# Kernel optimization log

Measured on AMD Instinct MI355X. Metric: run time of the kernel, lower is better.

Reference implementation:

```python
import jax, jax.numpy as jnp
import numpy as np

B, S, E, H, V = 1024, 64, 100, 512, 50000


def _gru_backward_last(x, wih, whh, bih, bhh):
    # x: [B,S,E]; PyTorch GRU cell, reverse direction; return final hidden [B,H]
    def step(h, xt):
        gi = xt @ wih.T + bih          # [B,3H]
        gh = h @ whh.T + bhh           # [B,3H]
        ir, iz, i_n = jnp.split(gi, 3, axis=-1)
        hr, hz, h_n = jnp.split(gh, 3, axis=-1)
        r = jax.nn.sigmoid(ir + hr)
        z = jax.nn.sigmoid(iz + hz)
        n = jnp.tanh(i_n + r * h_n)
        return (1.0 - z) * n + z * h, None
    h0 = jnp.zeros((x.shape[0], whh.shape[1]), x.dtype)
    hT, _ = jax.lax.scan(step, h0, x.transpose(1, 0, 2), reverse=True)
    return hT


def _encode(tokens, emb, wih, whh, bih, bhh):
    return _gru_backward_last(emb[tokens], wih, whh, bih, bhh)


def setup_inputs() -> dict:
    key = jax.random.key(0)
    ks = jax.random.split(key, 32)
    d = {}
    d['query'] = jax.random.randint(ks[0], (B, S), 0, V)
    d['context'] = jax.random.randint(ks[1], (B, S), 0, V)
    d['reply'] = jax.random.randint(ks[2], (B, S), 0, V)
    i = 3
    for tag in ('q', 'c', 'r'):
        d[f'emb_{tag}'] = jax.random.uniform(ks[i], (V, E), jnp.float32, -0.25, 0.25); i += 1
        d[f'wih_{tag}'] = jax.random.normal(ks[i], (3 * H, E), jnp.float32) * 0.05; i += 1
        d[f'whh_{tag}'] = jax.random.normal(ks[i], (3 * H, H), jnp.float32) * 0.05; i += 1
        d[f'bih_{tag}'] = jnp.zeros((3 * H,), jnp.float32); i += 1
        d[f'bhh_{tag}'] = jnp.zeros((3 * H,), jnp.float32); i += 1
    d['lin_w'] = jax.random.normal(ks[i], (H, H), jnp.float32) * 0.02
    d['lin_b'] = jnp.zeros((H,), jnp.float32)
    return d


def reference(query, context, reply,
              emb_q, wih_q, whh_q, bih_q, bhh_q,
              emb_c, wih_c, whh_c, bih_c, bhh_c,
              emb_r, wih_r, whh_r, bih_r, bhh_r,
              lin_w, lin_b):
    eq = _encode(query, emb_q, wih_q, whh_q, bih_q, bhh_q)    # [B,H]
    ec = _encode(context, emb_c, wih_c, whh_c, bih_c, bhh_c)  # [B,H]
    er = _encode(reply, emb_r, wih_r, whh_r, bih_r, bhh_r)    # [B,H]
    eqc = ((eq + ec) * 0.5) @ lin_w.T + lin_b                  # [B,H]
    sim = lambda a: jax.nn.softmax(a @ er.T, axis=-1)          # [B,B]
    return sim(eq), sim(ec), sim(eqc)
```

## Files before the change

kernel.cpp:

```cpp
#include <hip/hip_runtime.h>

typedef unsigned short u16;
typedef __attribute__((ext_vector_type(8))) short short8;
typedef __attribute__((ext_vector_type(4))) float f32x4;

#define B_   1024
#define S_   64
#define E_   100
#define H_   512
#define G3_  1536
#define XW_  256
#define WSZG (32 * 3 * 40 * 512)
#define GS_  (40 * 512)

__device__ __forceinline__ float bf2f(u16 u) {
    union { unsigned int u; float f; } c; c.u = ((unsigned int)u) << 16; return c.f;
}
__device__ __forceinline__ u16 f2bf(float f) {
    union { float f; unsigned int u; } c; c.f = f;
    unsigned int r = c.u + 0x7fffu + ((c.u >> 16) & 1u);
    return (u16)(r >> 16);
}
__device__ __forceinline__ f32x4 mfma16(short8 a, short8 b, f32x4 c) {
    return __builtin_amdgcn_mfma_f32_16x16x32_bf16(a, b, c, 0, 0, 0);
}

__global__ __launch_bounds__(256) void gather_kernel(
    const int* __restrict__ tok, const float* __restrict__ emb, u16* __restrict__ xs)
{
    int tid = threadIdx.x;
    int hw  = tid & 31;
    int rowid = blockIdx.x * 8 + (tid >> 5);
    int t = rowid >> 10, b = rowid & 1023;
    int token = tok[b * S_ + t];
    const float* src = emb + (long)token * E_;
    u16* dst = xs + (long)rowid * XW_;
    int c0 = hw * 4;
    u16 a1[4], a2[4];
    #pragma unroll
    for (int j = 0; j < 4; ++j) {
        int c = c0 + j;
        float v = (c < E_) ? src[c] : 0.f;
        u16 h = f2bf(v);
        a1[j] = h;
        a2[j] = f2bf(v - bf2f(h));
    }
    uint2 p1, p2;
    p1.x = (unsigned)a1[0] | ((unsigned)a1[1] << 16);
    p1.y = (unsigned)a1[2] | ((unsigned)a1[3] << 16);
    p2.x = (unsigned)a2[0] | ((unsigned)a2[1] << 16);
    p2.y = (unsigned)a2[2] | ((unsigned)a2[3] << 16);
    *(uint2*)(dst + c0)       = p1;
    *(uint2*)(dst + 128 + c0) = p2;
}

__global__ __launch_bounds__(256) void repack_swz(
    const float* __restrict__ wih, const float* __restrict__ whh, u16* __restrict__ out)
{
    long idx = (long)blockIdx.x * 256 + threadIdx.x;
    int jj   = idx & 7;
    int lane = (idx >> 3) & 63;
    int q9   = (int)(idx >> 9);
    int ks   = q9 % 40;
    int q    = q9 / 40;
    int gate = q % 3;
    int ht   = q / 3;
    int n   = ht * 16 + (lane & 15);
    int ck  = (lane >> 4) * 8 + jj;
    int row = gate * H_ + n;
    float w; int lo;
    if (ks < 8) {
        int kk = (ks & 3) * 32 + ck;
        if (kk >= E_) { out[idx] = 0; return; }
        w = wih[row * E_ + kk];
        lo = (ks >> 2);
    } else {
        int rel = ks - 8;
        int kk  = (rel & 15) * 32 + ck;
        w = whh[row * H_ + kk];
        lo = (rel >> 4);
    }
    u16 h = f2bf(w);
    if (lo) h = f2bf(w - bf2f(h));
    out[idx] = h;
}

__global__ __launch_bounds__(256) void repack_lin(
    const float* __restrict__ lw, u16* __restrict__ l1, u16* __restrict__ l2)
{
    int i = blockIdx.x * 256 + threadIdx.x;
    float w = lw[i];
    u16 h = f2bf(w);
    l1[i] = h;
    l2[i] = f2bf(w - bf2f(h));
}

struct BiasPtrs { const float* bih[3]; const float* bhh[3]; };

__global__ __launch_bounds__(256, 3) void gru_step(
    const u16* __restrict__ xs,
    const u16* __restrict__ wswz,
    BiasPtrs bp,
    const u16* __restrict__ h1_in, const u16* __restrict__ h2_in,
    u16* __restrict__ h1_out, u16* __restrict__ h2_out,
    int t)
{
    __shared__ __attribute__((aligned(16))) u16 As[2 * 64 * 72];
    const int tid = threadIdx.x;
    const int lane = tid & 63;
    const int kh = tid >> 7;
    const int nh = (tid >> 6) & 1;
    const int l15 = lane & 15, l4 = lane >> 4;
    const int htp = blockIdx.x;
    const int m0  = blockIdx.y * 64;
    const int g   = blockIdx.z;
    const int ht  = htp * 2 + nh;

    const u16* wg  = wswz + (long)g * WSZG + (long)ht * (3 * GS_) + lane * 8;
    const u16* xb  = xs + ((long)(g * S_ + t) * B_ + m0) * XW_;
    const u16* hb1 = h1_in + ((long)g * B_ + m0) * H_;
    const u16* hb2 = h2_in + ((long)g * B_ + m0) * H_;
    u16* slotp = As + kh * (64 * 72);

    f32x4 zero = {0.f, 0.f, 0.f, 0.f};
    f32x4 acc_r[4]  = {zero, zero, zero, zero};
    f32x4 acc_z[4]  = {zero, zero, zero, zero};
    f32x4 acc_ni[4] = {zero, zero, zero, zero};
    f32x4 acc_nh[4] = {zero, zero, zero, zero};

    auto stage2 = [&](const u16* s0, const u16* s1, int stride) {
        #pragma unroll
        for (int i = 0; i < 2; ++i) {
            int s = tid + 256 * i;
            int row = s >> 3, seg = s & 7;
            *(uint4*)(&As[row * 72 + seg * 8]) =
                *(const uint4*)(s0 + (long)row * stride + seg * 8);
            *(uint4*)(&As[64 * 72 + row * 72 + seg * 8]) =
                *(const uint4*)(s1 + (long)row * stride + seg * 8);
        }
    };
    auto consume_dual = [&](const u16* b1, const u16* b2, f32x4* accn) {
        #pragma unroll
        for (int ksl = 0; ksl < 2; ++ksl) {
            short8 br1 = *(const short8*)(b1 + ksl * 512);
            short8 bz1 = *(const short8*)(b1 + GS_ + ksl * 512);
            short8 bn1 = *(const short8*)(b1 + 2 * GS_ + ksl * 512);
            short8 br2 = *(const short8*)(b2 + ksl * 512);
            short8 bz2 = *(const short8*)(b2 + GS_ + ksl * 512);
            short8 bn2 = *(const short8*)(b2 + 2 * GS_ + ksl * 512);
            short8 a[4];
            #pragma unroll
            for (int q = 0; q < 4; ++q)
                a[q] = *(const short8*)(&slotp[(q * 16 + l15) * 72 + ksl * 32 + l4 * 8]);
            #pragma unroll
            for (int q = 0; q < 4; ++q) {
                acc_r[q] = mfma16(a[q], br1, acc_r[q]);
                acc_z[q] = mfma16(a[q], bz1, acc_z[q]);
                accn[q]  = mfma16(a[q], bn1, accn[q]);
                acc_r[q] = mfma16(a[q], br2, acc_r[q]);
                acc_z[q] = mfma16(a[q], bz2, acc_z[q]);
                accn[q]  = mfma16(a[q], bn2, accn[q]);
            }
        }
    };
    auto consume_single = [&](const u16* b1, f32x4* accn) {
        #pragma unroll
        for (int ksl = 0; ksl < 2; ++ksl) {
            short8 br1 = *(const short8*)(b1 + ksl * 512);
            short8 bz1 = *(const short8*)(b1 + GS_ + ksl * 512);
            short8 bn1 = *(const short8*)(b1 + 2 * GS_ + ksl * 512);
            short8 a[4];
            #pragma unroll
            for (int q = 0; q < 4; ++q)
                a[q] = *(const short8*)(&slotp[(q * 16 + l15) * 72 + ksl * 32 + l4 * 8]);
            #pragma unroll
            for (int q = 0; q < 4; ++q) {
                acc_r[q] = mfma16(a[q], br1, acc_r[q]);
                acc_z[q] = mfma16(a[q], bz1, acc_z[q]);
                accn[q]  = mfma16(a[q], bn1, accn[q]);
            }
        }
    };

    stage2(xb, xb + 64, XW_);
    __syncthreads();
    consume_dual(wg + (2 * kh) * 512, wg + (4 + 2 * kh) * 512, acc_ni);
    __syncthreads();
    stage2(xb + 128, xb + 192, XW_);
    __syncthreads();
    consume_single(wg + (2 * kh) * 512, acc_ni);
    __syncthreads();
    #pragma unroll 1
    for (int i = 0; i < 4; ++i) {
        stage2(hb1 + i * 64, hb1 + (i + 4) * 64, H_);
        __syncthreads();
        consume_dual(wg + (8 + 8 * kh + 2 * i) * 512,
                     wg + (24 + 8 * kh + 2 * i) * 512, acc_nh);
        __syncthreads();
    }
    #pragma unroll 1
    for (int i = 0; i < 4; ++i) {
        stage2(hb2 + i * 64, hb2 + (i + 4) * 64, H_);
        __syncthreads();
        consume_single(wg + (8 + 8 * kh + 2 * i) * 512, acc_nh);
        __syncthreads();
    }

    f32x4* rp = (f32x4*)As;
    const int ridx = (nh * 64 + lane) * 8;
    if (kh == 1) {
        #pragma unroll
        for (int q = 0; q < 4; ++q) { rp[ridx + q] = acc_r[q]; rp[ridx + 4 + q] = acc_z[q]; }
    }
    __syncthreads();
    if (kh == 0) {
        #pragma unroll
        for (int q = 0; q < 4; ++q) { acc_r[q] += rp[ridx + q]; acc_z[q] += rp[ridx + 4 + q]; }
    }
    __syncthreads();
    if (kh == 1) {
        #pragma unroll
        for (int q = 0; q < 4; ++q) { rp[ridx + q] = acc_ni[q]; rp[ridx + 4 + q] = acc_nh[q]; }
    }
    __syncthreads();
    if (kh == 0) {
        #pragma unroll
        for (int q = 0; q < 4; ++q) { acc_ni[q] += rp[ridx + q]; acc_nh[q] += rp[ridx + 4 + q]; }

        int hc = ht * 16 + l15;
        const float* bih = bp.bih[g];
        const float* bhh = bp.bhh[g];
        float b_ir = bih[hc],          b_hr = bhh[hc];
        float b_iz = bih[H_ + hc],     b_hz = bhh[H_ + hc];
        float b_in = bih[2 * H_ + hc], b_hn = bhh[2 * H_ + hc];
        #pragma unroll
        for (int mt = 0; mt < 4; ++mt) {
            #pragma unroll
            for (int i = 0; i < 4; ++i) {
                int m = m0 + mt * 16 + l4 * 4 + i;
                long idx = ((long)g * B_ + m) * H_ + hc;
                float pr = acc_r[mt][i] + b_ir + b_hr;
                float pz = acc_z[mt][i] + b_iz + b_hz;
                float vi = acc_ni[mt][i] + b_in;
                float vh = acc_nh[mt][i] + b_hn;
                float r = 1.f / (1.f + __expf(-pr));
                float z = 1.f / (1.f + __expf(-pz));
                float n = tanhf(vi + r * vh);
                float hold = bf2f(h1_in[idx]) + bf2f(h2_in[idx]);
                float hnew = (1.f - z) * n + z * hold;
                u16 hh = f2bf(hnew);
                h1_out[idx] = hh;
                h2_out[idx] = f2bf(hnew - bf2f(hh));
            }
        }
    }
}

__global__ __launch_bounds__(256) void qc_kernel(
    const u16* __restrict__ h1, const u16* __restrict__ h2,
    u16* __restrict__ q1, u16* __restrict__ q2)
{
    int i = blockIdx.x * 256 + threadIdx.x;
    float eq = bf2f(h1[i]) + bf2f(h2[i]);
    float ec = bf2f(h1[B_ * H_ + i]) + bf2f(h2[B_ * H_ + i]);
    float q = 0.5f * (eq + ec);
    u16 h = f2bf(q);
    q1[i] = h;
    q2[i] = f2bf(q - bf2f(h));
}

struct GArgs { const u16* a[24]; const u16* b[24]; };

__global__ __launch_bounds__(256) void gemm_nt(
    GArgs ga, int nch, int astr, int bstr,
    const float* __restrict__ bias, float* __restrict__ outf,
    u16* __restrict__ ohi, u16* __restrict__ olo, int ldc, int mode)
{
    __shared__ __attribute__((aligned(16))) u16 As[64 * 72];
    __shared__ __attribute__((aligned(16))) u16 Bs[64 * 72];
    const int tid = threadIdx.x;
    const int w = tid >> 6, lane = tid & 63;
    const int l15 = lane & 15, l4 = lane >> 4;
    const int m0 = blockIdx.x * 64, n0 = blockIdx.y * 64;

    f32x4 zero = {0.f, 0.f, 0.f, 0.f};
    f32x4 acc[4] = {zero, zero, zero, zero};

    for (int c = 0; c < nch; ++c) {
        int row = tid >> 2, seg = tid & 3;
        const u16* sa = ga.a[c] + (long)(m0 + row) * astr + seg * 16;
        *(uint4*)(&As[row * 72 + seg * 16])     = *(const uint4*)(sa);
        *(uint4*)(&As[row * 72 + seg * 16 + 8]) = *(const uint4*)(sa + 8);
        const u16* sb = ga.b[c] + (long)(n0 + row) * bstr + seg * 16;
        *(uint4*)(&Bs[row * 72 + seg * 16])     = *(const uint4*)(sb);
        *(uint4*)(&Bs[row * 72 + seg * 16 + 8]) = *(const uint4*)(sb + 8);
        __syncthreads();
        #pragma unroll
        for (int ks = 0; ks < 2; ++ks) {
            short8 bfrag = *(const short8*)(&Bs[(w * 16 + l15) * 72 + ks * 32 + l4 * 8]);
            #pragma unroll
            for (int rt = 0; rt < 4; ++rt) {
                short8 a = *(const short8*)(&As[(rt * 16 + l15) * 72 + ks * 32 + l4 * 8]);
                acc[rt] = mfma16(a, bfrag, acc[rt]);
            }
        }
        __syncthreads();
    }

    int n = n0 + w * 16 + l15;
    float bv = bias ? bias[n] : 0.f;
    #pragma unroll
    for (int rt = 0; rt < 4; ++rt) {
        #pragma unroll
        for (int i = 0; i < 4; ++i) {
            int m = m0 + rt * 16 + l4 * 4 + i;
            float v = acc[rt][i] + bv;
            if (mode == 0) {
                outf[(long)m * ldc + n] = v;
            } else {
                u16 h = f2bf(v);
                ohi[(long)m * ldc + n] = h;
                olo[(long)m * ldc + n] = f2bf(v - bf2f(h));
            }
        }
    }
}

__global__ __launch_bounds__(256) void softmax_kernel(
    const float* __restrict__ lg, float* __restrict__ out)
{
    __shared__ float red[256];
    int row = blockIdx.x, tid = threadIdx.x;
    const float* src = lg + (long)row * 1024;
    float x[4];
    float mx = -1e30f;
    #pragma unroll
    for (int i = 0; i < 4; ++i) { x[i] = src[tid + 256 * i]; mx = fmaxf(mx, x[i]); }
    red[tid] = mx; __syncthreads();
    for (int s = 128; s > 0; s >>= 1) { if (tid < s) red[tid] = fmaxf(red[tid], red[tid + s]); __syncthreads(); }
    mx = red[0]; __syncthreads();
    float sm = 0.f;
    #pragma unroll
    for (int i = 0; i < 4; ++i) { x[i] = __expf(x[i] - mx); sm += x[i]; }
    red[tid] = sm; __syncthreads();
    for (int s = 128; s > 0; s >>= 1) { if (tid < s) red[tid] += red[tid + s]; __syncthreads(); }
    float inv = 1.f / red[0];
    float* dst = out + (long)row * 1024;
    #pragma unroll
    for (int i = 0; i < 4; ++i) dst[tid + 256 * i] = x[i] * inv;
}

extern "C" void kernel_launch(void* const* d_in, const int* in_sizes, int n_in,
                              void* d_out, int out_size, void* d_ws, size_t ws_size,
                              hipStream_t stream)
{
    const int* tok[3] = {(const int*)d_in[0], (const int*)d_in[1], (const int*)d_in[2]};
    const float *emb[3], *wih[3], *whh[3], *bih[3], *bhh[3];
    for (int g = 0; g < 3; ++g) {
        emb[g] = (const float*)d_in[3 + 5 * g];
        wih[g] = (const float*)d_in[4 + 5 * g];
        whh[g] = (const float*)d_in[5 + 5 * g];
        bih[g] = (const float*)d_in[6 + 5 * g];
        bhh[g] = (const float*)d_in[7 + 5 * g];
    }
    const float* lin_w = (const float*)d_in[18];
    const float* lin_b = (const float*)d_in[19];

    char* ws = (char*)d_ws;
    size_t off = 0;
    auto alloc = [&](size_t bytes) { void* p = ws + off; off += (bytes + 255) & ~255ull; return p; };

    const size_t BH  = (size_t)B_ * H_;
    const size_t PRB = 3 * BH * 2;
    const size_t PING = 2 * PRB;

    u16*   Xs   = (u16*)alloc(3ll * S_ * B_ * XW_ * 2);
    u16*   Wswz = (u16*)alloc(3ll * WSZG * 2);
    u16*   LW1  = (u16*)alloc((size_t)H_ * H_ * 2);
    u16*   LW2  = (u16*)alloc((size_t)H_ * H_ * 2);
    char*  HB   = (char*)alloc(2 * PING);
    u16*   QC1  = (u16*)alloc(BH * 2);
    u16*   QC2  = (u16*)alloc(BH * 2);
    u16*   EQ1  = (u16*)alloc(BH * 2);
    u16*   EQ2  = (u16*)alloc(BH * 2);
    float* LG   = (float*)alloc(3ll * B_ * B_ * 4);

    u16* H1[2]; u16* H2[2];
    for (int i = 0; i < 2; ++i) {
        char* pb = HB + (size_t)i * PING;
        H1[i] = (u16*)pb;
        H2[i] = (u16*)(pb + PRB);
    }

    hipMemsetAsync(HB, 0, PING, stream);

    for (int g = 0; g < 3; ++g) {
        gather_kernel<<<dim3(S_ * B_ / 8), 256, 0, stream>>>(tok[g], emb[g], Xs + (size_t)g * S_ * B_ * XW_);
        repack_swz<<<dim3(WSZG / 256), 256, 0, stream>>>(wih[g], whh[g], Wswz + (size_t)g * WSZG);
    }
    repack_lin<<<dim3(H_ * H_ / 256), 256, 0, stream>>>(lin_w, LW1, LW2);

    BiasPtrs bp;
    for (int g = 0; g < 3; ++g) { bp.bih[g] = bih[g]; bp.bhh[g] = bhh[g]; }

    int p = 0;
    for (int t = S_ - 1; t >= 0; --t) {
        gru_step<<<dim3(16, 16, 3), 256, 0, stream>>>(Xs, Wswz, bp,
            H1[p], H2[p], H1[1 - p], H2[1 - p], t);
        p ^= 1;
    }
    const u16* H1F = H1[p];
    const u16* H2F = H2[p];

    qc_kernel<<<dim3(BH / 256), 256, 0, stream>>>(H1F, H2F, QC1, QC2);

    GArgs ga;
    for (int c = 0; c < 8; ++c)   { ga.a[c] = QC1 + c * 64;        ga.b[c] = LW1 + c * 64; }
    for (int c = 8; c < 16; ++c)  { ga.a[c] = QC2 + (c - 8) * 64;  ga.b[c] = LW1 + (c - 8) * 64; }
    for (int c = 16; c < 24; ++c) { ga.a[c] = QC1 + (c - 16) * 64; ga.b[c] = LW2 + (c - 16) * 64; }
    gemm_nt<<<dim3(16, 8), 256, 0, stream>>>(ga, 24, H_, H_, lin_b, nullptr, EQ1, EQ2, H_, 1);

    const u16* R1 = H1F + 2 * BH;
    const u16* R2 = H2F + 2 * BH;
    for (int g = 0; g < 3; ++g) {
        const u16 *A1, *A2;
        if (g == 0)      { A1 = H1F;      A2 = H2F; }
        else if (g == 1) { A1 = H1F + BH; A2 = H2F + BH; }
        else             { A1 = EQ1;      A2 = EQ2; }
        GArgs gs;
        for (int c = 0; c < 8; ++c)   { gs.a[c] = A1 + c * 64;        gs.b[c] = R1 + c * 64; }
        for (int c = 8; c < 16; ++c)  { gs.a[c] = A2 + (c - 8) * 64;  gs.b[c] = R1 + (c - 8) * 64; }
        for (int c = 16; c < 24; ++c) { gs.a[c] = A1 + (c - 16) * 64; gs.b[c] = R2 + (c - 16) * 64; }
        gemm_nt<<<dim3(16, 16), 256, 0, stream>>>(gs, 24, H_, H_, nullptr,
            LG + (size_t)g * B_ * B_, nullptr, nullptr, B_, 0);
    }

    softmax_kernel<<<dim3(3 * B_), 256, 0, stream>>>(LG, (float*)d_out);
}
```

Baseline: 2.260 ms.

## Double-buffer GRU step LDS staging with async global-to-LDS loads and swizzle

Replaces synchronous register-staged copies of the x and h tiles into padded shared memory with direct global_load_lds transfers into a double-buffered, XOR-swizzled LDS layout. The loop is fully unrolled so the next tile loads while the current one feeds MFMAs, halving the barrier count per chunk. The cross-wave reduction writes are also XOR-swizzled to reduce bank conflicts. This relies on correct implicit waitcnt before the barriers and doubles LDS usage, which may affect occupancy.

```diff
diff --git a/kernel.cpp b/kernel.cpp
--- a/kernel.cpp
+++ b/kernel.cpp
@@ -12,6 +12,9 @@
 #define XW_  256
 #define WSZG (32 * 3 * 40 * 512)
 #define GS_  (40 * 512)
+
+typedef __attribute__((address_space(1))) const unsigned int gu32;
+typedef __attribute__((address_space(3))) unsigned int lu32;
 
 __device__ __forceinline__ float bf2f(u16 u) {
     union { unsigned int u; float f; } c; c.u = ((unsigned int)u) << 16; return c.f;
@@ -105,9 +108,10 @@
     u16* __restrict__ h1_out, u16* __restrict__ h2_out,
     int t)
 {
-    __shared__ __attribute__((aligned(16))) u16 As[2 * 64 * 72];
+    __shared__ __attribute__((aligned(16))) u16 As[2][2][64 * 64];
     const int tid = threadIdx.x;
     const int lane = tid & 63;
+    const int wid = tid >> 6;
     const int kh = tid >> 7;
     const int nh = (tid >> 6) & 1;
     const int l15 = lane & 15, l4 = lane >> 4;
@@ -120,7 +124,6 @@
     const u16* xb  = xs + ((long)(g * S_ + t) * B_ + m0) * XW_;
     const u16* hb1 = h1_in + ((long)g * B_ + m0) * H_;
     const u16* hb2 = h2_in + ((long)g * B_ + m0) * H_;
-    u16* slotp = As + kh * (64 * 72);
 
     f32x4 zero = {0.f, 0.f, 0.f, 0.f};
     f32x4 acc_r[4]  = {zero, zero, zero, zero};
@@ -128,18 +131,27 @@
     f32x4 acc_ni[4] = {zero, zero, zero, zero};
     f32x4 acc_nh[4] = {zero, zero, zero, zero};
 
-    auto stage2 = [&](const u16* s0, const u16* s1, int stride) {
-        #pragma unroll
-        for (int i = 0; i < 2; ++i) {
-            int s = tid + 256 * i;
-            int row = s >> 3, seg = s & 7;
-            *(uint4*)(&As[row * 72 + seg * 8]) =
-                *(const uint4*)(s0 + (long)row * stride + seg * 8);
-            *(uint4*)(&As[64 * 72 + row * 72 + seg * 8]) =
-                *(const uint4*)(s1 + (long)row * stride + seg * 8);
+    auto stage_async = [&](int buf, const u16* s0, const u16* s1, int stride) {
+        #pragma unroll
+        for (int i = 0; i < 4; ++i) {
+            int seg  = wid * 4 + i;
+            int slot = seg >> 3;
+            int rblk = seg & 7;
+            const u16* src = slot ? s1 : s0;
+            int row = rblk * 8 + (lane >> 3);
+            int ch  = (lane & 7) ^ ((lane >> 3) & 7);
+            const u16* gp = src + (long)row * stride + ch * 8;
+            u16* lp = &As[buf][slot][rblk * 8 * 64];
+            __builtin_amdgcn_global_load_lds((gu32*)gp, (lu32*)lp, 16, 0, 0);
         }
     };
-    auto consume_dual = [&](const u16* b1, const u16* b2, f32x4* accn) {
+    auto ldA = [&](const u16* sp, int ksl, int q) -> short8 {
+        int r = q * 16 + l15;
+        int p = ((ksl << 2) + l4) ^ (l15 & 7);
+        return *(const short8*)(&sp[r * 64 + p * 8]);
+    };
+    auto consume_dual = [&](int buf, const u16* b1, const u16* b2, f32x4* accn) {
+        const u16* sp = &As[buf][kh][0];
         #pragma unroll
         for (int ksl = 0; ksl < 2; ++ksl) {
             short8 br1 = *(const short8*)(b1 + ksl * 512);
@@ -150,8 +162,7 @@
             short8 bn2 = *(const short8*)(b2 + 2 * GS_ + ksl * 512);
             short8 a[4];
             #pragma unroll
-            for (int q = 0; q < 4; ++q)
-                a[q] = *(const short8*)(&slotp[(q * 16 + l15) * 72 + ksl * 32 + l4 * 8]);
+            for (int q = 0; q < 4; ++q) a[q] = ldA(sp, ksl, q);
             #pragma unroll
             for (int q = 0; q < 4; ++q) {
                 acc_r[q] = mfma16(a[q], br1, acc_r[q]);
@@ -163,7 +174,8 @@
             }
         }
     };
-    auto consume_single = [&](const u16* b1, f32x4* accn) {
+    auto consume_single = [&](int buf, const u16* b1, f32x4* accn) {
+        const u16* sp = &As[buf][kh][0];
         #pragma unroll
         for (int ksl = 0; ksl < 2; ++ksl) {
             short8 br1 = *(const short8*)(b1 + ksl * 512);
@@ -171,8 +183,7 @@
             short8 bn1 = *(const short8*)(b1 + 2 * GS_ + ksl * 512);
             short8 a[4];
             #pragma unroll
-            for (int q = 0; q < 4; ++q)
-                a[q] = *(const short8*)(&slotp[(q * 16 + l15) * 72 + ksl * 32 + l4 * 8]);
+            for (int q = 0; q < 4; ++q) a[q] = ldA(sp, ksl, q);
             #pragma unroll
             for (int q = 0; q < 4; ++q) {
                 acc_r[q] = mfma16(a[q], br1, acc_r[q]);
@@ -182,50 +193,70 @@
         }
     };
 
-    stage2(xb, xb + 64, XW_);
-    __syncthreads();
-    consume_dual(wg + (2 * kh) * 512, wg + (4 + 2 * kh) * 512, acc_ni);
-    __syncthreads();
-    stage2(xb + 128, xb + 192, XW_);
-    __syncthreads();
-    consume_single(wg + (2 * kh) * 512, acc_ni);
-    __syncthreads();
-    #pragma unroll 1
-    for (int i = 0; i < 4; ++i) {
-        stage2(hb1 + i * 64, hb1 + (i + 4) * 64, H_);
-        __syncthreads();
-        consume_dual(wg + (8 + 8 * kh + 2 * i) * 512,
-                     wg + (24 + 8 * kh + 2 * i) * 512, acc_nh);
-        __syncthreads();
-    }
-    #pragma unroll 1
-    for (int i = 0; i < 4; ++i) {
-        stage2(hb2 + i * 64, hb2 + (i + 4) * 64, H_);
-        __syncthreads();
-        consume_single(wg + (8 + 8 * kh + 2 * i) * 512, acc_nh);
-        __syncthreads();
-    }
+    stage_async(0, xb, xb + 64, XW_);
+    __syncthreads();
+    stage_async(1, xb + 128, xb + 192, XW_);
+    consume_dual(0, wg + (2 * kh) * 512, wg + (4 + 2 * kh) * 512, acc_ni);
+    __syncthreads();
+    stage_async(0, hb1, hb1 + 4 * 64, H_);
+    consume_single(1, wg + (2 * kh) * 512, acc_ni);
+    __syncthreads();
+    stage_async(1, hb1 + 1 * 64, hb1 + 5 * 64, H_);
+    consume_dual(0, wg + (8 + 8 * kh + 0) * 512, wg + (24 + 8 * kh + 0) * 512, acc_nh);
+    __syncthreads();
+    stage_async(0, hb1 + 2 * 64, hb1 + 6 * 64, H_);
+    consume_dual(1, wg + (8 + 8 * kh + 2) * 512, wg + (24 + 8 * kh + 2) * 512, acc_nh);
+    __syncthreads();
+    stage_async(1, hb1 + 3 * 64, hb1 + 7 * 64, H_);
+    consume_dual(0, wg + (8 + 8 * kh + 4) * 512, wg + (24 + 8 * kh + 4) * 512, acc_nh);
+    __syncthreads();
+    stage_async(0, hb2, hb2 + 4 * 64, H_);
+    consume_dual(1, wg + (8 + 8 * kh + 6) * 512, wg + (24 + 8 * kh + 6) * 512, acc_nh);
+    __syncthreads();
+    stage_async(1, hb2 + 1 * 64, hb2 + 5 * 64, H_);
+    consume_single(0, wg + (8 + 8 * kh + 0) * 512, acc_nh);
+    __syncthreads();
+    stage_async(0, hb2 + 2 * 64, hb2 + 6 * 64, H_);
+    consume_single(1, wg + (8 + 8 * kh + 2) * 512, acc_nh);
+    __syncthreads();
+    stage_async(1, hb2 + 3 * 64, hb2 + 7 * 64, H_);
+    consume_single(0, wg + (8 + 8 * kh + 4) * 512, acc_nh);
+    __syncthreads();
+    consume_single(1, wg + (8 + 8 * kh + 6) * 512, acc_nh);
 
     f32x4* rp = (f32x4*)As;
-    const int ridx = (nh * 64 + lane) * 8;
+    const int rbase = (nh * 64 + lane) * 8;
+    const int rxor  = lane & 7;
     if (kh == 1) {
         #pragma unroll
-        for (int q = 0; q < 4; ++q) { rp[ridx + q] = acc_r[q]; rp[ridx + 4 + q] = acc_z[q]; }
+        for (int q = 0; q < 4; ++q) {
+            rp[rbase + (q ^ rxor)]       = acc_r[q];
+            rp[rbase + ((4 + q) ^ rxor)] = acc_z[q];
+        }
     }
     __syncthreads();
     if (kh == 0) {
         #pragma unroll
-        for (int q = 0; q < 4; ++q) { acc_r[q] += rp[ridx + q]; acc_z[q] += rp[ridx + 4 + q]; }
+        for (int q = 0; q < 4; ++q) {
+            acc_r[q] += rp[rbase + (q ^ rxor)];
+            acc_z[q] += rp[rbase + ((4 + q) ^ rxor)];
+        }
     }
     __syncthreads();
     if (kh == 1) {
         #pragma unroll
-        for (int q = 0; q < 4; ++q) { rp[ridx + q] = acc_ni[q]; rp[ridx + 4 + q] = acc_nh[q]; }
+        for (int q = 0; q < 4; ++q) {
+            rp[rbase + (q ^ rxor)]       = acc_ni[q];
+            rp[rbase + ((4 + q) ^ rxor)] = acc_nh[q];
+        }
     }
     __syncthreads();
     if (kh == 0) {
         #pragma unroll
-        for (int q = 0; q < 4; ++q) { acc_ni[q] += rp[ridx + q]; acc_nh[q] += rp[ridx + 4 + q]; }
+        for (int q = 0; q < 4; ++q) {
+            acc_ni[q] += rp[rbase + (q ^ rxor)];
+            acc_nh[q] += rp[rbase + ((4 + q) ^ rxor)];
+        }
 
         int hc = ht * 16 + l15;
         const float* bih = bp.bih[g];
```

Result: faster. 2.121 ms (-6.2%).
